# Performance work log

Measured on AMD Instinct MI355X. Metric: run time of the kernel, lower is better.

Reference implementation:

```python
import jax, jax.numpy as jnp
import numpy as np

B, L, C, PS, K, NL, NH, DFF, MAXLEN = 64, 4096, 32, 16, 1024, 4, 8, 2048, 512
D = PS * C          # code_dim = 512
P = L // PS         # num_patches = 256
PA_H = 4            # heads in PatchCrossAttention (largest of {4,2,1} dividing C)
COMMIT = 0.25


def _ln(x, g, b, eps=1e-5):
    m = x.mean(-1, keepdims=True)
    v = x.var(-1, keepdims=True)
    return (x - m) / jnp.sqrt(v + eps) * g + b


def _mha(q, k, v, w_in, b_in, w_out, b_out, nh, mask=None):
    # torch nn.MultiheadAttention math: in_proj weight [3d, d], y = x @ W.T + b
    d = q.shape[-1]
    dh = d // nh
    wq, wk, wv = jnp.split(w_in, 3, axis=0)
    bq, bk, bv = jnp.split(b_in, 3, axis=0)
    qh = (q @ wq.T + bq).reshape(q.shape[0], q.shape[1], nh, dh)
    kh = (k @ wk.T + bk).reshape(k.shape[0], k.shape[1], nh, dh)
    vh = (v @ wv.T + bv).reshape(v.shape[0], v.shape[1], nh, dh)
    scores = jnp.einsum('bqhd,bkhd->bhqk', qh, kh) / jnp.sqrt(jnp.asarray(dh, q.dtype))
    if mask is not None:
        scores = jnp.where(mask, jnp.asarray(-jnp.inf, scores.dtype), scores)
    a = jax.nn.softmax(scores, axis=-1)
    o = jnp.einsum('bhqk,bkhd->bqhd', a, vh).reshape(q.shape[0], q.shape[1], d)
    return o @ w_out.T + b_out


def _forward(x, pa_lq, pa_pos, pa_win, pa_bin, pa_wout, pa_bout,
             pa_ln1g, pa_ln1b, pa_ln2g, pa_ln2b, pa_w1, pa_b1, pa_w2, pa_b2,
             cb, tf_pos, tf_win, tf_bin, tf_wout, tf_bout,
             tf_ln1g, tf_ln1b, tf_ln2g, tf_ln2b,
             tf_w1, tf_b1, tf_w2, tf_b2, fin_g, fin_b):
    Bx = x.shape[0]
    # --- patchify: [B, L, C] -> [B*P, PS, C] ---
    xp = x.reshape(Bx * P, PS, C)
    # --- PatchCrossAttention ---
    x_pos = xp + pa_pos                       # pos emb over patch steps
    lq = jnp.broadcast_to(pa_lq, xp.shape)    # learnable query tokens
    attn = _mha(lq, x_pos, x_pos, pa_win, pa_bin, pa_wout, pa_bout, PA_H)
    xn = _ln(lq + attn, pa_ln1g, pa_ln1b)
    f = jax.nn.gelu(xn @ pa_w1 + pa_b1, approximate=False) @ pa_w2 + pa_b2
    xo = _ln(xn + f, pa_ln2g, pa_ln2b)
    enc = xp + xo                             # residual to raw patch
    # --- flatten + VQ ---
    z = enc.reshape(Bx * P, D)
    d2 = (z * z).sum(1, keepdims=True) + (cb * cb).sum(1) - 2.0 * (z @ cb.T)
    idx = jnp.argmin(d2, axis=1)
    q = cb[idx]
    sg = jax.lax.stop_gradient
    e_loss = jnp.mean((sg(q) - z) ** 2)
    q_loss = jnp.mean((q - sg(z)) ** 2)
    vq_loss = q_loss + COMMIT * e_loss
    quant = z + sg(q - z)                     # straight-through
    # --- causal transformer over code sequence [B, P, D] ---
    t = quant.reshape(Bx, P, D) + tf_pos[:P]
    causal = jnp.triu(jnp.ones((P, P), dtype=bool), 1)
    for i in range(NL):  # post-LN TransformerEncoderLayer, gelu
        a = _mha(t, t, t, tf_win[i], tf_bin[i], tf_wout[i], tf_bout[i], NH, causal)
        t = _ln(t + a, tf_ln1g[i], tf_ln1b[i])
        f = jax.nn.gelu(t @ tf_w1[i] + tf_b1[i], approximate=False) @ tf_w2[i] + tf_b2[i]
        t = _ln(t + f, tf_ln2g[i], tf_ln2b[i])
    y = _ln(t, fin_g, fin_b)
    return y, vq_loss, idx


def setup_inputs() -> dict:
    key = jax.random.key(0)
    ks = iter(jax.random.split(key, 32))
    n = lambda shape, s=0.02: jax.random.normal(next(ks), shape, dtype=jnp.float32) * s
    inp = {
        'x': jax.random.normal(next(ks), (B, L, C), dtype=jnp.float32),
        'pa_lq': n((PS, C)), 'pa_pos': n((PS, C)),
        'pa_win': n((3 * C, C)), 'pa_bin': jnp.zeros((3 * C,), jnp.float32),
        'pa_wout': n((C, C)), 'pa_bout': jnp.zeros((C,), jnp.float32),
        'pa_ln1g': jnp.ones((C,), jnp.float32), 'pa_ln1b': jnp.zeros((C,), jnp.float32),
        'pa_ln2g': jnp.ones((C,), jnp.float32), 'pa_ln2b': jnp.zeros((C,), jnp.float32),
        'pa_w1': n((C, 2 * C)), 'pa_b1': jnp.zeros((2 * C,), jnp.float32),
        'pa_w2': n((2 * C, C)), 'pa_b2': jnp.zeros((C,), jnp.float32),
        'cb': jax.random.uniform(next(ks), (K, D), jnp.float32, -1.0 / K, 1.0 / K),
        'tf_pos': n((MAXLEN, D)),
        'tf_win': n((NL, 3 * D, D)), 'tf_bin': jnp.zeros((NL, 3 * D), jnp.float32),
        'tf_wout': n((NL, D, D)), 'tf_bout': jnp.zeros((NL, D), jnp.float32),
        'tf_ln1g': jnp.ones((NL, D), jnp.float32), 'tf_ln1b': jnp.zeros((NL, D), jnp.float32),
        'tf_ln2g': jnp.ones((NL, D), jnp.float32), 'tf_ln2b': jnp.zeros((NL, D), jnp.float32),
        'tf_w1': n((NL, D, DFF)), 'tf_b1': jnp.zeros((NL, DFF), jnp.float32),
        'tf_w2': n((NL, DFF, D)), 'tf_b2': jnp.zeros((NL, D), jnp.float32),
        'fin_g': jnp.ones((D,), jnp.float32), 'fin_b': jnp.zeros((D,), jnp.float32),
    }
    return inp


def reference(x, pa_lq, pa_pos, pa_win, pa_bin, pa_wout, pa_bout,
              pa_ln1g, pa_ln1b, pa_ln2g, pa_ln2b, pa_w1, pa_b1, pa_w2, pa_b2,
              cb, tf_pos, tf_win, tf_bin, tf_wout, tf_bout,
              tf_ln1g, tf_ln1b, tf_ln2g, tf_ln2b,
              tf_w1, tf_b1, tf_w2, tf_b2, fin_g, fin_b):
    return _forward(x, pa_lq, pa_pos, pa_win, pa_bin, pa_wout, pa_bout,
                    pa_ln1g, pa_ln1b, pa_ln2g, pa_ln2b, pa_w1, pa_b1, pa_w2, pa_b2,
                    cb, tf_pos, tf_win, tf_bin, tf_wout, tf_bout,
                    tf_ln1g, tf_ln1b, tf_ln2g, tf_ln2b,
                    tf_w1, tf_b1, tf_w2, tf_b2, fin_g, fin_b)
```

## Files before the change

kernel.cpp:

```cpp
#include <hip/hip_runtime.h>


#define SQRT1_2F 0.70710678118654752440f

typedef __attribute__((ext_vector_type(8))) short short8;
typedef __attribute__((ext_vector_type(4))) float f32x4;
typedef __attribute__((ext_vector_type(8))) unsigned short ushort8;
typedef unsigned short ushort;
typedef unsigned long long u64;

__device__ __forceinline__ float gelu_exact(float v) {
  return 0.5f * v * (1.0f + erff(v * SQRT1_2F));
}

__device__ __forceinline__ ushort f2b_rne(float f) {
  unsigned u = __float_as_uint(f);
  unsigned r = (u + 0x7fffu + ((u >> 16) & 1u)) >> 16;
  return (ushort)r;
}

__device__ __forceinline__ float b2f(ushort u) {
  return __uint_as_float(((unsigned)u) << 16);
}

__device__ __forceinline__ void gload16(const void* g, void* l) {
  __builtin_amdgcn_global_load_lds(
      (const __attribute__((address_space(1))) void*)g,
      (__attribute__((address_space(3))) void*)l, 16, 0, 0);
}

__device__ __forceinline__ unsigned fkey(float d) {
  unsigned u = __float_as_uint(d);
  return (u & 0x80000000u) ? ~u : (u | 0x80000000u);
}

__global__ __launch_bounds__(64) void patch_setup_kernel(
    const float* __restrict__ lq, const float* __restrict__ win,
    const float* __restrict__ bin, const float* __restrict__ w1,
    const float* __restrict__ w2, float* __restrict__ q16,
    float* __restrict__ w1T, float* __restrict__ w2T) {
  const int tid = threadIdx.x;
#pragma unroll
  for (int q = 0; q < 8; q++) {
    int e = tid + (q << 6);
    int i = e >> 5, c = e & 31;
    const float* wr = win + (size_t)c * 32;
    float acc = bin[c];
#pragma unroll
    for (int d = 0; d < 32; d++) acc += lq[(i << 5) + d] * wr[d];
    q16[e] = acc;
  }
#pragma unroll
  for (int q = 0; q < 32; q++) {
    int e = tid + (q << 6);
    int u = e >> 5, d = e & 31;
    w1T[e] = w1[(size_t)d * 64 + u];
  }
#pragma unroll
  for (int q = 0; q < 32; q++) {
    int e = tid + (q << 6);
    int c = e >> 6, u = e & 63;
    w2T[e] = w2[(size_t)u * 32 + c];
  }
}

__device__ __forceinline__ void ln_16xS(float* buf, const float* g,
                                        const float* bb, int tid) {
  int row = tid >> 2, sub = tid & 3;
  int c0 = sub << 3;
  float* r = buf + row * 34 + c0;
  float v[8];
  float s = 0.f, s2 = 0.f;
#pragma unroll
  for (int n = 0; n < 8; n++) {
    float t = r[n];
    v[n] = t; s += t; s2 += t * t;
  }
  s += __shfl_xor(s, 1);  s += __shfl_xor(s, 2);
  s2 += __shfl_xor(s2, 1); s2 += __shfl_xor(s2, 2);
  float m = s * (1.0f / 32.0f);
  float var = s2 * (1.0f / 32.0f) - m * m;
  float inv = 1.0f / sqrtf(var + 1e-5f);
#pragma unroll
  for (int n = 0; n < 8; n++)
    r[n] = (v[n] - m) * inv * g[c0 + n] + bb[c0 + n];
}

__global__ __launch_bounds__(256) void pkF_kernel(
    const float* __restrict__ x, const float* __restrict__ pos,
    const float* __restrict__ win, const float* __restrict__ bin,
    const float* __restrict__ q16,
    const float* __restrict__ wout, const float* __restrict__ bout,
    const float* __restrict__ lq,
    const float* __restrict__ ln1g, const float* __restrict__ ln1b,
    const float* __restrict__ w1T, const float* __restrict__ b1,
    const float* __restrict__ w2T, const float* __restrict__ b2,
    const float* __restrict__ ln2g, const float* __restrict__ ln2b,
    float* __restrict__ z, ushort* __restrict__ zh,
    ushort* __restrict__ zl, float* __restrict__ znorm) {
  __shared__ float sso[2176];
  __shared__ float ubuf[6672];
  float* sxp  = ubuf;
  float* skv  = ubuf + 2048;
  float* sq16 = ubuf + 6144;
  float* sstA = ubuf;
  float* sshA = ubuf + 2176;

  const int blk = blockIdx.x, t = threadIdx.x;
  const int p0 = blk << 2;
  const int cfix = t & 31;
  const int wv = t >> 6, lane = t & 63;

#pragma unroll
  for (int q = 0; q < 8; q++) {
    int e = t + (q << 8);
    int pl = e >> 9, r = e & 511;
    sxp[e] = x[(size_t)(p0 + pl) * 512 + r] + pos[r];
  }
  if (t < 128) {
#pragma unroll
    for (int q = 0; q < 4; q++) {
      int e = t + (q << 7);
      sq16[(e >> 5) * 33 + (e & 31)] = q16[e];
    }
  }

  float wr0[32], wr1[32];
#pragma unroll
  for (int d4 = 0; d4 < 8; d4++) {
    *(float4*)(wr0 + 4 * d4) =
        *(const float4*)(win + (size_t)(32 + cfix) * 32 + 4 * d4);
    *(float4*)(wr1 + 4 * d4) =
        *(const float4*)(win + (size_t)(64 + cfix) * 32 + 4 * d4);
  }
  const float bk = bin[32 + cfix];
  const float bvv = bin[64 + cfix];
  __syncthreads();

#pragma unroll
  for (int q = 0; q < 16; q++) {
    int e = t + (q << 8);
    int pl = e >> 10, rr = e & 1023;
    int w = rr >> 9, rj = rr & 511, j = rj >> 5;
    const float* sx = sxp + (pl << 9) + (j << 5);
    const float* wreg = w ? wr1 : wr0;
    float acc = w ? bvv : bk;
#pragma unroll
    for (int d = 0; d < 32; d++) acc += sx[d] * wreg[d];
    skv[e] = acc;
  }
  __syncthreads();

  {
    const int pl = t >> 6, hh = (t >> 4) & 3, i = t & 15;
    const float* kp = skv + (pl << 10);
    const int hd = hh << 3;

    float sc[16];
#pragma unroll
    for (int j = 0; j < 16; j++) {
      float acc = 0.f;
#pragma unroll
      for (int d = 0; d < 8; d++)
        acc += sq16[i * 33 + hd + d] * kp[(j << 5) + hd + d];
      sc[j] = acc * 0.35355339059327373f;
    }
    {
      float mx = sc[0];
#pragma unroll
      for (int j = 1; j < 16; j++) mx = fmaxf(mx, sc[j]);
      float sm = 0.f;
      float ev[16];
#pragma unroll
      for (int j = 0; j < 16; j++) { ev[j] = expf(sc[j] - mx); sm += ev[j]; }
      float inv = 1.0f / sm;
#pragma unroll
      for (int j = 0; j < 16; j++) sc[j] = ev[j] * inv;
    }
    float* orow = sso + pl * 544 + i * 34 + hd;
#pragma unroll
    for (int c8 = 0; c8 < 8; c8++) {
      const int c = hd + c8;
      float acc = 0.f;
#pragma unroll
      for (int j = 0; j < 16; j++) acc += sc[j] * kp[512 + (j << 5) + c];
      orow[c8] = acc;
    }
  }
  __syncthreads();

  const int p = p0 + wv;
  float* psso = sso + wv * 544;
  float* psst = sstA + wv * 544;
  float* pssh = sshA + wv * 1056;

  float wo[32];
#pragma unroll
  for (int d4 = 0; d4 < 8; d4++)
    *(float4*)(wo + 4 * d4) = *(const float4*)(wout + (size_t)cfix * 32 + 4 * d4);

#pragma unroll
  for (int q = 0; q < 8; q++) {
    int e = lane + (q << 6);
    int i = e >> 5;
    float acc = bout[cfix];
#pragma unroll
    for (int d = 0; d < 32; d++) acc += psso[i * 34 + d] * wo[d];
    psst[i * 34 + cfix] = acc + lq[(i << 5) + cfix];
  }
  __syncthreads();
  ln_16xS(psst, ln1g, ln1b, lane);

  float w1r[32];
#pragma unroll
  for (int d4 = 0; d4 < 8; d4++)
    *(float4*)(w1r + 4 * d4) = *(const float4*)(w1T + (size_t)lane * 32 + 4 * d4);
  __syncthreads();

#pragma unroll
  for (int q = 0; q < 16; q++) {
    int i = q;
    float acc = b1[lane];
#pragma unroll
    for (int d = 0; d < 32; d++) acc += psst[i * 34 + d] * w1r[d];
    pssh[i * 66 + lane] = gelu_exact(acc);
  }

  float w2r[64];
#pragma unroll
  for (int u4 = 0; u4 < 16; u4++)
    *(float4*)(w2r + 4 * u4) = *(const float4*)(w2T + (size_t)cfix * 64 + 4 * u4);
  __syncthreads();

#pragma unroll
  for (int q = 0; q < 8; q++) {
    int e = lane + (q << 6);
    int i = e >> 5;
    float acc = b2[cfix];
#pragma unroll
    for (int u = 0; u < 64; u++) acc += pssh[i * 66 + u] * w2r[u];
    psso[i * 34 + cfix] = acc + psst[i * 34 + cfix];
  }
  __syncthreads();
  ln_16xS(psso, ln2g, ln2b, lane);
  __syncthreads();

  const float* xp = x + (size_t)p * 512;
  const int row = lane >> 2, c0v = (lane & 3) << 3;
  float zv[8];
#pragma unroll
  for (int n = 0; n < 8; n++)
    zv[n] = xp[(lane << 3) + n] + psso[row * 34 + c0v + n];
  float* zo = z + (size_t)p * 512 + (lane << 3);
  *(float4*)(zo)     = *(float4*)(zv);
  *(float4*)(zo + 4) = *(float4*)(zv + 4);
  ushort8 hv, lv;
  float s2 = 0.f;
#pragma unroll
  for (int n = 0; n < 8; n++) {
    s2 += zv[n] * zv[n];
    ushort h = f2b_rne(zv[n]);
    hv[n] = h;
    lv[n] = f2b_rne(zv[n] - b2f(h));
  }
  *(ushort8*)(zh + (size_t)p * 512 + (lane << 3)) = hv;
  *(ushort8*)(zl + (size_t)p * 512 + (lane << 3)) = lv;
#pragma unroll
  for (int off = 1; off < 64; off <<= 1) s2 += __shfl_xor(s2, off);
  if (lane == 0) znorm[p] = s2;
}

__global__ __launch_bounds__(64) void cbnorm_kernel(
    const float* __restrict__ cb, float* __restrict__ cbn,
    ushort* __restrict__ ch, ushort* __restrict__ cl) {
  int c = blockIdx.x, lane = threadIdx.x;
  const float* r = cb + (size_t)c * 512 + lane * 8;
  float v[8];
  *(float4*)(v)     = *(const float4*)(r);
  *(float4*)(v + 4) = *(const float4*)(r + 4);
  float s = 0.f;
  ushort8 hv, lv;
#pragma unroll
  for (int n = 0; n < 8; n++) {
    s += v[n] * v[n];
    ushort h = f2b_rne(v[n]);
    hv[n] = h;
    lv[n] = f2b_rne(v[n] - b2f(h));
  }
  *(ushort8*)(ch + (size_t)c * 512 + lane * 8) = hv;
  *(ushort8*)(cl + (size_t)c * 512 + lane * 8) = lv;
#pragma unroll
  for (int off = 1; off < 64; off <<= 1) s += __shfl_xor(s, off);
  if (lane == 0) cbn[c] = s;
}

__global__ __launch_bounds__(256) void gemm_vq_b3(
    const ushort* __restrict__ Ah, const ushort* __restrict__ Al,
    const ushort* __restrict__ Bh, const ushort* __restrict__ Bl,
    const float* __restrict__ znorm, const float* __restrict__ cbn,
    u64* __restrict__ packed) {
  __shared__ ushort sAh[4096], sAl[4096], sBh[4096], sBl[4096];
  const int cpx = gridDim.x >> 3;
  const int bid = (blockIdx.x & 7) * cpx + (blockIdx.x >> 3);
  const int bx = bid & 7, by = bid >> 3;
  const int m0 = by << 7, n0 = bx << 7;
  const int tid = threadIdx.x;
  const int wid = tid >> 6, lane = tid & 63;
  const int wr = wid >> 1, wc = wid & 1;
  const int l15 = lane & 15, lk = lane >> 4;

  const f32x4 fzero = {0.f, 0.f, 0.f, 0.f};
  f32x4 acc[4][4];
#pragma unroll
  for (int i = 0; i < 4; i++)
#pragma unroll
    for (int j = 0; j < 4; j++) acc[i][j] = fzero;

  for (int k0 = 0; k0 < 512; k0 += 32) {
#pragma unroll
    for (int c = 0; c < 2; c++) {
      const int I = tid + (c << 8);
      const int r = I >> 2, kk = (I & 3) << 3;
      const size_t ga = (size_t)(m0 + r) * 512 + k0 + kk;
      const size_t gb = (size_t)(n0 + r) * 512 + k0 + kk;
      const size_t lo = (size_t)((wid << 6) + (c << 8)) * 8;
      gload16(Ah + ga, sAh + lo);
      gload16(Al + ga, sAl + lo);
      gload16(Bh + gb, sBh + lo);
      gload16(Bl + gb, sBl + lo);
    }
    __syncthreads();

    short8 ah[4], al[4], bh[4], bl[4];
#pragma unroll
    for (int m = 0; m < 4; m++) {
      const int ar = ((wr << 6) + (m << 4) + l15) * 32 + lk * 8;
      ah[m] = *(const short8*)(sAh + ar);
      al[m] = *(const short8*)(sAl + ar);
      const int br = ((wc << 6) + (m << 4) + l15) * 32 + lk * 8;
      bh[m] = *(const short8*)(sBh + br);
      bl[m] = *(const short8*)(sBl + br);
    }
#pragma unroll
    for (int m = 0; m < 4; m++)
#pragma unroll
      for (int n = 0; n < 4; n++) {
        acc[m][n] = __builtin_amdgcn_mfma_f32_16x16x32_bf16(ah[m], bh[n],
                                                            acc[m][n], 0, 0, 0);
        acc[m][n] = __builtin_amdgcn_mfma_f32_16x16x32_bf16(ah[m], bl[n],
                                                            acc[m][n], 0, 0, 0);
        acc[m][n] = __builtin_amdgcn_mfma_f32_16x16x32_bf16(al[m], bh[n],
                                                            acc[m][n], 0, 0, 0);
      }
    __syncthreads();
  }

  float zn[4][4];
#pragma unroll
  for (int m = 0; m < 4; m++)
#pragma unroll
    for (int r = 0; r < 4; r++)
      zn[m][r] = znorm[m0 + (wr << 6) + (m << 4) + (lk << 2) + r];
  float cbnv[4];
#pragma unroll
  for (int n = 0; n < 4; n++)
    cbnv[n] = cbn[n0 + (wc << 6) + (n << 4) + l15];

#pragma unroll
  for (int m = 0; m < 4; m++) {
#pragma unroll
    for (int r = 0; r < 4; r++) {
      u64 best = ~0ull;
#pragma unroll
      for (int n = 0; n < 4; n++) {
        const int gcol = n0 + (wc << 6) + (n << 4) + l15;
        float d = (zn[m][r] + cbnv[n]) - 2.0f * acc[m][n][r];
        u64 key = ((u64)fkey(d) << 32) | (unsigned)gcol;
        best = best < key ? best : key;
      }
#pragma unroll
      for (int off = 1; off < 16; off <<= 1) {
        u64 o = __shfl_xor(best, off);
        best = best < o ? best : o;
      }
      if (l15 == 0) {
        const int grow = m0 + (wr << 6) + (m << 4) + (lk << 2) + r;
        atomicMin(&packed[grow], best);
      }
    }
  }
}

__global__ __launch_bounds__(256) void vq_slim_kernel(
    const u64* __restrict__ packed, const float* __restrict__ cb,
    const float* __restrict__ z, const float* __restrict__ tf_pos,
    ushort* __restrict__ th,
    float* __restrict__ idx_out, float* __restrict__ loss_part) {
  __shared__ float spart[4];
  const int wv = threadIdx.x >> 6;
  const int r = (blockIdx.x << 2) + wv;
  const int lane = threadIdx.x & 63;
  const int bi = (int)(unsigned)(packed[r] & 0xFFFFFFFFull);
  const float* zr = z + (size_t)r * 512 + (lane << 3);
  const float* q = cb + (size_t)bi * 512 + (lane << 3);
  const float* pr = tf_pos + (size_t)(r & 255) * 512 + (lane << 3);
  float zv[8], qv[8], pv[8];
  *(float4*)(zv)     = *(const float4*)(zr);
  *(float4*)(zv + 4) = *(const float4*)(zr + 4);
  *(float4*)(qv)     = *(const float4*)(q);
  *(float4*)(qv + 4) = *(const float4*)(q + 4);
  *(float4*)(pv)     = *(const float4*)(pr);
  *(float4*)(pv + 4) = *(const float4*)(pr + 4);
  float lsum = 0.f;
  ushort8 w;
#pragma unroll
  for (int n = 0; n < 8; n++) {
    float diff = qv[n] - zv[n];
    lsum += diff * diff;
    w[n] = f2b_rne(qv[n] + pv[n]);
  }
  *(ushort8*)(th + (size_t)r * 512 + (lane << 3)) = w;
#pragma unroll
  for (int off = 1; off < 64; off <<= 1) lsum += __shfl_xor(lsum, off);
  if (lane == 0) {
    idx_out[r] = (float)bi;
    spart[wv] = lsum;
  }
  __syncthreads();
  if (threadIdx.x == 0)
    loss_part[blockIdx.x] = (spart[0] + spart[1]) + (spart[2] + spart[3]);
}

__global__ __launch_bounds__(256) void loss_reduce_kernel(
    const float* __restrict__ loss_part, float* __restrict__ loss_out) {
  __shared__ float sw[4];
  float s = 0.f;
  for (int i = threadIdx.x; i < 4096; i += 256) s += loss_part[i];
#pragma unroll
  for (int off = 1; off < 64; off <<= 1) s += __shfl_xor(s, off);
  const int wv = threadIdx.x >> 6;
  if ((threadIdx.x & 63) == 0) sw[wv] = s;
  __syncthreads();
  if (threadIdx.x == 0)
    loss_out[0] = ((sw[0] + sw[1]) + (sw[2] + sw[3])) * (1.25f / 8388608.0f);
}

template <int OUTMODE>
__global__ __launch_bounds__(256) void gemm_bf16_kernel(
    const ushort* __restrict__ A, const ushort* __restrict__ B,
    const float* __restrict__ bias, void* __restrict__ Cout,
    int M, int N, int K) {
  __shared__ ushort As[8192];
  __shared__ ushort Bs[8192];
  const int nbx = N >> 7;
  const int cpx = gridDim.x >> 3;
  const int bid = (blockIdx.x & 7) * cpx + (blockIdx.x >> 3);
  const int bx = bid % nbx, by = bid / nbx;
  const int m0 = by << 7, n0 = bx << 7;
  const int tid = threadIdx.x;
  const int wid = tid >> 6, lane = tid & 63;
  const int wr = wid >> 1, wc = wid & 1;
  const int l15 = lane & 15, lk = lane >> 4;

  const f32x4 fzero = {0.f, 0.f, 0.f, 0.f};
  f32x4 acc[4][4];
#pragma unroll
  for (int i = 0; i < 4; i++)
#pragma unroll
    for (int j = 0; j < 4; j++) acc[i][j] = fzero;

  for (int k0 = 0; k0 < K; k0 += 64) {
#pragma unroll
    for (int c = 0; c < 4; c++) {
      const int base = (c << 8) + (wid << 6);
      const int half = base >> 9;
      const int Jb = base & 511;
      const int J = Jb + lane;
      const int r = J >> 2, kk = (J & 3) << 3;
      gload16(A + (size_t)(m0 + r) * K + k0 + (half << 5) + kk,
              As + (size_t)((half << 12) + Jb * 8));
      gload16(B + (size_t)(n0 + r) * K + k0 + (half << 5) + kk,
              Bs + (size_t)((half << 12) + Jb * 8));
    }
    __syncthreads();

#pragma unroll
    for (int kc = 0; kc < 2; kc++) {
      short8 a[4], b[4];
#pragma unroll
      for (int m = 0; m < 4; m++) {
        const int ar = (kc << 12) + ((wr << 6) + (m << 4) + l15) * 32 + lk * 8;
        a[m] = *(const short8*)(As + ar);
        const int br = (kc << 12) + ((wc << 6) + (m << 4) + l15) * 32 + lk * 8;
        b[m] = *(const short8*)(Bs + br);
      }
#pragma unroll
      for (int m = 0; m < 4; m++)
#pragma unroll
        for (int n = 0; n < 4; n++)
          acc[m][n] = __builtin_amdgcn_mfma_f32_16x16x32_bf16(a[m], b[n],
                                                              acc[m][n], 0, 0, 0);
    }
    __syncthreads();
  }

  float bv[4];
#pragma unroll
  for (int n = 0; n < 4; n++)
    bv[n] = bias[n0 + (wc << 6) + (n << 4) + l15];

#pragma unroll
  for (int m = 0; m < 4; m++) {
#pragma unroll
    for (int n = 0; n < 4; n++) {
      const int gcol = n0 + (wc << 6) + (n << 4) + l15;
#pragma unroll
      for (int r = 0; r < 4; r++) {
        const int grow = m0 + (wr << 6) + (m << 4) + (lk << 2) + r;
        float v = acc[m][n][r] + bv[n];
        if (OUTMODE == 0) {
          ((float*)Cout)[(size_t)grow * N + gcol] = v;
        } else if (OUTMODE == 1) {
          ((ushort*)Cout)[(size_t)grow * N + gcol] = f2b_rne(gelu_exact(v));
        } else {
          ((ushort*)Cout)[(size_t)grow * N + gcol] = f2b_rne(v);
        }
      }
    }
  }
}

__global__ void cvt_flat(const float* __restrict__ in, ushort* __restrict__ out,
                         int n) {
  int i = blockIdx.x * blockDim.x + threadIdx.x;
  const int stride = gridDim.x * blockDim.x;
  for (; i < n; i += stride) out[i] = f2b_rne(in[i]);
}

__global__ __launch_bounds__(256) void cvt_tr(const float* __restrict__ in,
                                              ushort* __restrict__ out,
                                              int R, int C) {
  __shared__ float tile[32][33];
  const int bc = blockIdx.x, br = blockIdx.y, lay = blockIdx.z;
  const float* src = in + (size_t)lay * R * C;
  ushort* dst = out + (size_t)lay * R * C;
  const int tid = threadIdx.x;
#pragma unroll
  for (int q = 0; q < 4; q++) {
    int idx = tid + (q << 8);
    int rr = idx >> 5, cc = idx & 31;
    tile[rr][cc] = src[(size_t)(br * 32 + rr) * C + bc * 32 + cc];
  }
  __syncthreads();
#pragma unroll
  for (int q = 0; q < 4; q++) {
    int idx = tid + (q << 8);
    int co = idx >> 5, ro = idx & 31;
    dst[(size_t)(bc * 32 + co) * R + br * 32 + ro] = f2b_rne(tile[ro][co]);
  }
}

__global__ __launch_bounds__(64) void attn_mfma_kernel(
    const ushort* __restrict__ qkv, ushort* __restrict__ o) {
  __shared__ ushort lds[8192];
  char* KsB = (char*)lds;
  char* VtB = (char*)(lds + 4096);
  const int bid = blockIdx.x;
  const int xcd = bid & 7, slot = bid >> 3;
  const int b = (xcd << 3) | (slot >> 5);
  const int h = (slot >> 2) & 7;
  const int qb = slot & 3;
  const int lane = threadIdx.x;
  const int l15 = lane & 15, lk4 = lane >> 4;

  short8 qf[4][2];
#pragma unroll
  for (int m = 0; m < 4; m++)
#pragma unroll
    for (int kc = 0; kc < 2; kc++)
      qf[m][kc] = *(const short8*)(qkv +
          (size_t)(b * 256 + qb * 64 + m * 16 + l15) * 1536 +
          h * 64 + kc * 32 + lk4 * 8);

  const f32x4 fz = {0.f, 0.f, 0.f, 0.f};
  f32x4 O[4][4];
#pragma unroll
  for (int m = 0; m < 4; m++)
#pragma unroll
    for (int n = 0; n < 4; n++) O[m][n] = fz;
  float lsum[4][4];
#pragma unroll
  for (int m = 0; m < 4; m++)
#pragma unroll
    for (int r = 0; r < 4; r++) lsum[m][r] = 0.f;

  ushort8 kv[8], vv[8];
  {
    const ushort* krow = qkv + (size_t)(b * 256 + lane) * 1536 + 512 + h * 64;
#pragma unroll
    for (int u = 0; u < 8; u++) kv[u] = ((const ushort8*)krow)[u];
#pragma unroll
    for (int u = 0; u < 8; u++) vv[u] = ((const ushort8*)(krow + 512))[u];
  }

  for (int jt = 0; jt <= qb; jt++) {
    __syncthreads();
    {
      const int rx = (lane & 7) << 4;
#pragma unroll
      for (int u = 0; u < 8; u++)
        *(ushort8*)(KsB + lane * 128 + ((u << 4) ^ rx)) = kv[u];
#pragma unroll
      for (int u = 0; u < 8; u++)
#pragma unroll
        for (int i = 0; i < 8; i++) {
          const int d = u * 8 + i;
          *(ushort*)(VtB + ((d * 128 + lane * 2) ^ ((d & 7) << 4))) =
              (ushort)vv[u][i];
        }
    }
    __syncthreads();

    if (jt < qb) {
      const ushort* krow = qkv +
          (size_t)(b * 256 + (jt + 1) * 64 + lane) * 1536 + 512 + h * 64;
#pragma unroll
      for (int u = 0; u < 8; u++) kv[u] = ((const ushort8*)krow)[u];
#pragma unroll
      for (int u = 0; u < 8; u++) vv[u] = ((const ushort8*)(krow + 512))[u];
    }

    f32x4 sacc[4][4];
#pragma unroll
    for (int m = 0; m < 4; m++)
#pragma unroll
      for (int n = 0; n < 4; n++) sacc[m][n] = fz;
    __builtin_amdgcn_s_setprio(1);
#pragma unroll
    for (int kc = 0; kc < 2; kc++) {
      short8 bf[4];
#pragma unroll
      for (int n = 0; n < 4; n++) {
        const int row = n * 16 + l15;
        bf[n] = *(const short8*)(KsB + row * 128 +
                                 ((kc * 64 + lk4 * 16) ^ ((row & 7) << 4)));
      }
#pragma unroll
      for (int m = 0; m < 4; m++)
#pragma unroll
        for (int n = 0; n < 4; n++)
          sacc[m][n] = __builtin_amdgcn_mfma_f32_16x16x32_bf16(
              qf[m][kc], bf[n], sacc[m][n], 0, 0, 0);
    }
    __builtin_amdgcn_s_setprio(0);
    __syncthreads();

    const bool diag = (jt == qb);
#pragma unroll
    for (int m = 0; m < 4; m++)
#pragma unroll
      for (int n = 0; n < 4; n++)
#pragma unroll
        for (int r = 0; r < 4; r++) {
          const int ql = m * 16 + lk4 * 4 + r;
          const int jl = n * 16 + l15;
          float e = __expf(sacc[m][n][r] * 0.125f);
          if (diag && jl > ql) e = 0.f;
          const ushort pu = f2b_rne(e);
          lsum[m][r] += b2f(pu);
          *(ushort*)(KsB + ql * 128 + ((jl * 2) ^ ((ql & 7) << 4))) = pu;
        }
    __syncthreads();

    __builtin_amdgcn_s_setprio(1);
#pragma unroll
    for (int kc = 0; kc < 2; kc++) {
      short8 pf[4], vf[4];
#pragma unroll
      for (int m = 0; m < 4; m++) {
        const int row = m * 16 + l15;
        pf[m] = *(const short8*)(KsB + row * 128 +
                                 ((kc * 64 + lk4 * 16) ^ ((row & 7) << 4)));
      }
#pragma unroll
      for (int n = 0; n < 4; n++) {
        const int row = n * 16 + l15;
        vf[n] = *(const short8*)(VtB + row * 128 +
                                 ((kc * 64 + lk4 * 16) ^ ((row & 7) << 4)));
      }
#pragma unroll
      for (int m = 0; m < 4; m++)
#pragma unroll
        for (int n = 0; n < 4; n++)
          O[m][n] = __builtin_amdgcn_mfma_f32_16x16x32_bf16(
              pf[m], vf[n], O[m][n], 0, 0, 0);
    }
    __builtin_amdgcn_s_setprio(0);
  }

  float inv[4][4];
#pragma unroll
  for (int m = 0; m < 4; m++)
#pragma unroll
    for (int r = 0; r < 4; r++) {
      float v = lsum[m][r];
      v += __shfl_xor(v, 1); v += __shfl_xor(v, 2);
      v += __shfl_xor(v, 4); v += __shfl_xor(v, 8);
      inv[m][r] = 1.0f / v;
    }
#pragma unroll
  for (int m = 0; m < 4; m++)
#pragma unroll
    for (int n = 0; n < 4; n++)
#pragma unroll
      for (int r = 0; r < 4; r++) {
        const int row = b * 256 + qb * 64 + m * 16 + lk4 * 4 + r;
        const int col = h * 64 + n * 16 + l15;
        o[(size_t)row * 512 + col] = f2b_rne(O[m][n][r] * inv[m][r]);
      }
}

__global__ __launch_bounds__(256) void ln_kernel(
    const ushort* __restrict__ xin_b, const ushort* __restrict__ addin_b,
    const float* __restrict__ g, const float* __restrict__ bb,
    ushort* __restrict__ outb, float* __restrict__ outp) {
  const int r = blockIdx.x * 4 + (threadIdx.x >> 6);
  const int lane = threadIdx.x & 63;
  ushort8 xv = *(const ushort8*)(xin_b + (size_t)r * 512 + lane * 8);
  float v[8];
#pragma unroll
  for (int n = 0; n < 8; n++) v[n] = b2f(xv[n]);
  if (addin_b) {
    ushort8 a = *(const ushort8*)(addin_b + (size_t)r * 512 + lane * 8);
#pragma unroll
    for (int n = 0; n < 8; n++) v[n] += b2f(a[n]);
  }
  float s = 0.f, s2 = 0.f;
#pragma unroll
  for (int n = 0; n < 8; n++) { s += v[n]; s2 += v[n] * v[n]; }
#pragma unroll
  for (int off = 1; off < 64; off <<= 1) {
    s += __shfl_xor(s, off);
    s2 += __shfl_xor(s2, off);
  }
  float m = s * (1.0f / 512.0f);
  float var = s2 * (1.0f / 512.0f) - m * m;
  float inv = 1.0f / sqrtf(var + 1e-5f);
  const int c0 = lane * 8;
  float outv[8];
#pragma unroll
  for (int n = 0; n < 8; n++) outv[n] = (v[n] - m) * inv * g[c0 + n] + bb[c0 + n];
  if (outb) {
    ushort8 w;
#pragma unroll
    for (int n = 0; n < 8; n++) w[n] = f2b_rne(outv[n]);
    *(ushort8*)(outb + (size_t)r * 512 + c0) = w;
  }
  if (outp) {
    float* orow = outp + (size_t)r * 512 + c0;
    *(float4*)(orow)     = *(float4*)(outv);
    *(float4*)(orow + 4) = *(float4*)(outv + 4);
  }
}

extern "C" void kernel_launch(void* const* d_in, const int* in_sizes, int n_in,
                              void* d_out, int out_size, void* d_ws, size_t ws_size,
                              hipStream_t stream) {
  const float* x       = (const float*)d_in[0];
  const float* pa_lq   = (const float*)d_in[1];
  const float* pa_pos  = (const float*)d_in[2];
  const float* pa_win  = (const float*)d_in[3];
  const float* pa_bin  = (const float*)d_in[4];
  const float* pa_wout = (const float*)d_in[5];
  const float* pa_bout = (const float*)d_in[6];
  const float* pa_ln1g = (const float*)d_in[7];
  const float* pa_ln1b = (const float*)d_in[8];
  const float* pa_ln2g = (const float*)d_in[9];
  const float* pa_ln2b = (const float*)d_in[10];
  const float* pa_w1   = (const float*)d_in[11];
  const float* pa_b1   = (const float*)d_in[12];
  const float* pa_w2   = (const float*)d_in[13];
  const float* pa_b2   = (const float*)d_in[14];
  const float* cb      = (const float*)d_in[15];
  const float* tf_pos  = (const float*)d_in[16];
  const float* tf_win  = (const float*)d_in[17];
  const float* tf_bin  = (const float*)d_in[18];
  const float* tf_wout = (const float*)d_in[19];
  const float* tf_bout = (const float*)d_in[20];
  const float* tf_ln1g = (const float*)d_in[21];
  const float* tf_ln1b = (const float*)d_in[22];
  const float* tf_ln2g = (const float*)d_in[23];
  const float* tf_ln2b = (const float*)d_in[24];
  const float* tf_w1   = (const float*)d_in[25];
  const float* tf_b1   = (const float*)d_in[26];
  const float* tf_w2   = (const float*)d_in[27];
  const float* tf_b2   = (const float*)d_in[28];
  const float* fin_g   = (const float*)d_in[29];
  const float* fin_b   = (const float*)d_in[30];

  float* yout = (float*)d_out;
  float* loss_out = yout + 8388608;
  float* idx_out = loss_out + 1;

  float* ws   = (float*)d_ws;
  float* z    = ws;
  float* tb   = z + 8388608;
  float* bufA = tb + 8388608;
  float* bufC = bufA + 16777216;
  float* wreg = bufC + 8388608;
  float* treg = wreg + 6291456;
  float* cbn  = treg + 4194304;
  float* q16  = cbn + 1024;
  float* w1T  = q16 + 512;
  float* w2T  = w1T + 2048;
  float* znorm = w2T + 2048;
  u64*   packed = (u64*)(znorm + 16384);
  float* loss_part = (float*)(packed + 16384);

  ushort* win_b  = (ushort*)wreg;
  ushort* wout_b = win_b + 3145728;
  ushort* w1t_b  = wout_b + 1048576;
  ushort* w2t_b  = w1t_b + 4194304;
  ushort* tbh    = (ushort*)treg;
  ushort* qkvh   = (ushort*)bufA;
  ushort* abh    = (ushort*)z;
  ushort* zh_b   = (ushort*)bufC;
  ushort* zl_b   = zh_b + 8388608;
  ushort* projh  = (ushort*)bufC;
  ushort* ch_b   = (ushort*)treg;
  ushort* cl_b   = ch_b + 524288;

  hipMemsetAsync(packed, 0xFF, 16384 * sizeof(u64), stream);
  cbnorm_kernel<<<1024, 64, 0, stream>>>(cb, cbn, ch_b, cl_b);
  patch_setup_kernel<<<1, 64, 0, stream>>>(pa_lq, pa_win, pa_bin, pa_w1,
                                           pa_w2, q16, w1T, w2T);

  pkF_kernel<<<4096, 256, 0, stream>>>(x, pa_pos, pa_win, pa_bin, q16,
                                       pa_wout, pa_bout, pa_lq,
                                       pa_ln1g, pa_ln1b, w1T, pa_b1,
                                       w2T, pa_b2, pa_ln2g, pa_ln2b,
                                       z, zh_b, zl_b, znorm);

  cvt_flat<<<2048, 256, 0, stream>>>(tf_win, win_b, 3145728);
  cvt_flat<<<1024, 256, 0, stream>>>(tf_wout, wout_b, 1048576);
  cvt_tr<<<dim3(64, 16, 4), 256, 0, stream>>>(tf_w1, w1t_b, 512, 2048);
  cvt_tr<<<dim3(16, 64, 4), 256, 0, stream>>>(tf_w2, w2t_b, 2048, 512);

  gemm_vq_b3<<<dim3(1024), 256, 0, stream>>>(zh_b, zl_b, ch_b, cl_b,
                                             znorm, cbn, packed);
  vq_slim_kernel<<<4096, 256, 0, stream>>>(packed, cb, z, tf_pos, tbh,
                                           idx_out, loss_part);
  loss_reduce_kernel<<<1, 256, 0, stream>>>(loss_part, loss_out);

  for (int l = 0; l < 4; l++) {
    gemm_bf16_kernel<2><<<dim3(128 * 12), 256, 0, stream>>>(
        tbh, win_b + (size_t)l * 1536 * 512, tf_bin + l * 1536, qkvh,
        16384, 1536, 512);
    attn_mfma_kernel<<<dim3(2048), 64, 0, stream>>>(qkvh, abh);
    gemm_bf16_kernel<2><<<dim3(128 * 4), 256, 0, stream>>>(
        abh, wout_b + (size_t)l * 512 * 512, tf_bout + l * 512, projh,
        16384, 512, 512);
    ln_kernel<<<dim3(4096), 256, 0, stream>>>(tbh, projh, tf_ln1g + l * 512,
                                              tf_ln1b + l * 512, tbh, nullptr);
    gemm_bf16_kernel<1><<<dim3(128 * 16), 256, 0, stream>>>(
        tbh, w1t_b + (size_t)l * 1048576, tf_b1 + l * 2048, qkvh,
        16384, 2048, 512);
    gemm_bf16_kernel<2><<<dim3(128 * 4), 256, 0, stream>>>(
        qkvh, w2t_b + (size_t)l * 1048576, tf_b2 + l * 512, projh,
        16384, 512, 2048);
    ln_kernel<<<dim3(4096), 256, 0, stream>>>(tbh, projh, tf_ln2g + l * 512,
                                              tf_ln2b + l * 512, tbh, nullptr);
  }
  ln_kernel<<<dim3(4096), 256, 0, stream>>>(tbh, nullptr, fin_g, fin_b,
                                            nullptr, yout);

  (void)in_sizes; (void)n_in; (void)out_size; (void)ws_size;
}
```

Baseline: 1.228 ms.

## Drop fp32 z buffer in favor of bf16 hi/lo split and stage attention output via LDS

The patch encoder no longer writes an fp32 copy of z. The VQ loss kernel rebuilds z from the existing bf16 hi/lo split buffers, which removes one full fp32 write and read of a 16384x512 tensor. Separately, the attention kernel now stages its output tile in LDS and writes coalesced 16-byte rows instead of scattered 2-byte stores. The hi+lo reconstruction slightly changes the precision of the commitment loss, and the LDS reuse assumes the attention tiles are no longer needed at that point.

```diff
diff --git a/kernel.cpp b/kernel.cpp
--- a/kernel.cpp
+++ b/kernel.cpp
@@ -96,8 +96,8 @@
     const float* __restrict__ w1T, const float* __restrict__ b1,
     const float* __restrict__ w2T, const float* __restrict__ b2,
     const float* __restrict__ ln2g, const float* __restrict__ ln2b,
-    float* __restrict__ z, ushort* __restrict__ zh,
-    ushort* __restrict__ zl, float* __restrict__ znorm) {
+    ushort* __restrict__ zh, ushort* __restrict__ zl,
+    float* __restrict__ znorm) {
   __shared__ float sso[2176];
   __shared__ float ubuf[6672];
   float* sxp  = ubuf;
@@ -251,9 +251,6 @@
 #pragma unroll
   for (int n = 0; n < 8; n++)
     zv[n] = xp[(lane << 3) + n] + psso[row * 34 + c0v + n];
-  float* zo = z + (size_t)p * 512 + (lane << 3);
-  *(float4*)(zo)     = *(float4*)(zv);
-  *(float4*)(zo + 4) = *(float4*)(zv + 4);
   ushort8 hv, lv;
   float s2 = 0.f;
 #pragma unroll
@@ -393,20 +390,19 @@
 
 __global__ __launch_bounds__(256) void vq_slim_kernel(
     const u64* __restrict__ packed, const float* __restrict__ cb,
-    const float* __restrict__ z, const float* __restrict__ tf_pos,
-    ushort* __restrict__ th,
+    const ushort* __restrict__ zh, const ushort* __restrict__ zl,
+    const float* __restrict__ tf_pos, ushort* __restrict__ th,
     float* __restrict__ idx_out, float* __restrict__ loss_part) {
   __shared__ float spart[4];
   const int wv = threadIdx.x >> 6;
   const int r = (blockIdx.x << 2) + wv;
   const int lane = threadIdx.x & 63;
   const int bi = (int)(unsigned)(packed[r] & 0xFFFFFFFFull);
-  const float* zr = z + (size_t)r * 512 + (lane << 3);
+  ushort8 hv = *(const ushort8*)(zh + (size_t)r * 512 + (lane << 3));
+  ushort8 lv = *(const ushort8*)(zl + (size_t)r * 512 + (lane << 3));
   const float* q = cb + (size_t)bi * 512 + (lane << 3);
   const float* pr = tf_pos + (size_t)(r & 255) * 512 + (lane << 3);
-  float zv[8], qv[8], pv[8];
-  *(float4*)(zv)     = *(const float4*)(zr);
-  *(float4*)(zv + 4) = *(const float4*)(zr + 4);
+  float qv[8], pv[8];
   *(float4*)(qv)     = *(const float4*)(q);
   *(float4*)(qv + 4) = *(const float4*)(q + 4);
   *(float4*)(pv)     = *(const float4*)(pr);
@@ -415,7 +411,8 @@
   ushort8 w;
 #pragma unroll
   for (int n = 0; n < 8; n++) {
-    float diff = qv[n] - zv[n];
+    float zv = b2f(hv[n]) + b2f(lv[n]);
+    float diff = qv[n] - zv;
     lsum += diff * diff;
     w[n] = f2b_rne(qv[n] + pv[n]);
   }
@@ -708,16 +705,25 @@
       v += __shfl_xor(v, 4); v += __shfl_xor(v, 8);
       inv[m][r] = 1.0f / v;
     }
+
+  ushort* Ob = lds;
 #pragma unroll
   for (int m = 0; m < 4; m++)
 #pragma unroll
     for (int n = 0; n < 4; n++)
 #pragma unroll
       for (int r = 0; r < 4; r++) {
-        const int row = b * 256 + qb * 64 + m * 16 + lk4 * 4 + r;
-        const int col = h * 64 + n * 16 + l15;
-        o[(size_t)row * 512 + col] = f2b_rne(O[m][n][r] * inv[m][r]);
-      }
+        const int row = m * 16 + lk4 * 4 + r;
+        const int col = n * 16 + l15;
+        Ob[row * 66 + col] = f2b_rne(O[m][n][r] * inv[m][r]);
+      }
+#pragma unroll
+  for (int it = 0; it < 8; it++) {
+    const int row = it * 8 + (lane >> 3);
+    const int c0 = (lane & 7) << 3;
+    ushort8 w = *(const ushort8*)(Ob + row * 66 + c0);
+    *(ushort8*)(o + (size_t)(b * 256 + qb * 64 + row) * 512 + h * 64 + c0) = w;
+  }
 }
 
 __global__ __launch_bounds__(256) void ln_kernel(
@@ -839,7 +845,7 @@
                                        pa_wout, pa_bout, pa_lq,
                                        pa_ln1g, pa_ln1b, w1T, pa_b1,
                                        w2T, pa_b2, pa_ln2g, pa_ln2b,
-                                       z, zh_b, zl_b, znorm);
+                                       zh_b, zl_b, znorm);
 
   cvt_flat<<<2048, 256, 0, stream>>>(tf_win, win_b, 3145728);
   cvt_flat<<<1024, 256, 0, stream>>>(tf_wout, wout_b, 1048576);
@@ -848,8 +854,8 @@
 
   gemm_vq_b3<<<dim3(1024), 256, 0, stream>>>(zh_b, zl_b, ch_b, cl_b,
                                              znorm, cbn, packed);
-  vq_slim_kernel<<<4096, 256, 0, stream>>>(packed, cb, z, tf_pos, tbh,
-                                           idx_out, loss_part);
+  vq_slim_kernel<<<4096, 256, 0, stream>>>(packed, cb, zh_b, zl_b, tf_pos,
+                                           tbh, idx_out, loss_part);
   loss_reduce_kernel<<<1, 256, 0, stream>>>(loss_part, loss_out);
 
   for (int l = 0; l < 4; l++) {
```

Result: faster. 1.187 ms (median of 2 runs) (-3.4%).
